# Performance work log

Measured on AMD Instinct MI355X. Metric: run time of the kernel, lower is better.

Reference implementation:

```python
import jax, jax.numpy as jnp
import numpy as np

jax.config.update("jax_enable_x64", True)  # original casts to double for cov/cholesky

B, C, H, W, DR = 64, 2048, 14, 14, 256
EPS = 1e-6      # LCMCOV eps added to covariance diagonal
BN_EPS = 1e-5   # torch BatchNorm2d default eps


def setup_inputs() -> dict:
    key = jax.random.key(0)
    k0, k1 = jax.random.split(key)
    x = jax.random.normal(k0, (B, C, H, W), dtype=jnp.float32)
    # 1x1 conv weight (kaiming fan_out for relu): std = sqrt(2 / fan_out), fan_out = DR*1*1... torch uses fan_out = out_ch*k*k per output; approximate with sqrt(2/C) scale on (DR, C)
    w_conv = jax.random.normal(k1, (DR, C), dtype=jnp.float32) * np.sqrt(2.0 / C).astype(np.float32)
    gamma = jnp.ones((DR,), jnp.float32)
    beta = jnp.zeros((DR,), jnp.float32)
    run_mean = jnp.zeros((DR,), jnp.float32)
    run_var = jnp.ones((DR,), jnp.float32)
    return {"x": x, "w_conv": w_conv, "gamma": gamma, "beta": beta,
            "run_mean": run_mean, "run_var": run_var}


def reference(x, w_conv, gamma, beta, run_mean, run_var):
    b, c, h, w = x.shape
    dr = w_conv.shape[0]
    m = h * w
    # 1x1 conv (no bias) + BatchNorm2d (eval mode, running stats) + ReLU
    y = jnp.einsum('bchw,dc->bdhw', x, w_conv)
    scale = gamma / jnp.sqrt(run_var + BN_EPS)
    y = y * scale[None, :, None, None] + (beta - run_mean * scale)[None, :, None, None]
    y = jax.nn.relu(y)
    # Covpool in float64: x I_hat x^T == (1/M) * (x - mean)(x - mean)^T
    xd = y.reshape(b, dr, m).astype(jnp.float64)
    xc = xd - xd.mean(axis=2, keepdims=True)  # [B, DR, M]
    cov = jnp.einsum('bdm,bem->bde', xc, xc) / m  # [B, DR, DR]
    # LogI_LCM: Cholesky, log the diagonal, symmetrize
    cov = cov + EPS * jnp.eye(dr, dtype=jnp.float64)
    L = jnp.linalg.cholesky(cov)
    diag = jnp.log(jnp.diagonal(L, axis1=-2, axis2=-1))          # [B, DR]
    tril = jnp.tril(L, -1) + jnp.eye(dr, dtype=L.dtype) * diag[:, :, None]
    sym = tril + jnp.swapaxes(tril, -1, -2)
    # Triuvec: upper-triangular (incl diag) entries in row-major order, cast to float32
    iu, ju = jnp.triu_indices(dr)
    return sym[:, iu, ju].astype(jnp.float32)  # [B, DR*(DR+1)/2]
```

## Files before the change

kernel.cpp:

```cpp
#include <hip/hip_runtime.h>
#include <math.h>

#define BB 64
#define CC 2048
#define MM 196
#define DD 256
#define NTOT (BB * MM)

typedef __attribute__((ext_vector_type(8))) short short8;
typedef __attribute__((ext_vector_type(4))) short short4v;
typedef __attribute__((ext_vector_type(4))) unsigned short ushort4v;
typedef __attribute__((ext_vector_type(4))) float f32x4;

__device__ __forceinline__ unsigned short bf16_rne(float f) {
  unsigned int u = __float_as_uint(f);
  unsigned int r = u + 0x7FFFu + ((u >> 16) & 1u);
  return (unsigned short)(r >> 16);
}

__global__ __launch_bounds__(256) void k_prep(
    const float* __restrict__ w, const float* __restrict__ gamma,
    const float* __restrict__ beta, const float* __restrict__ rmean,
    const float* __restrict__ rvar, unsigned short* __restrict__ wh,
    unsigned short* __restrict__ wl, float* __restrict__ sclv,
    float* __restrict__ sftv) {
  const int e0 = (blockIdx.x * 256 + threadIdx.x) * 4;
  f32x4 v = *(const f32x4*)(w + e0);
  ushort4v h, l;
#pragma unroll
  for (int i = 0; i < 4; ++i) {
    unsigned short hb = bf16_rne(v[i]);
    float hf = __uint_as_float((unsigned int)hb << 16);
    h[i] = hb;
    l[i] = bf16_rne(v[i] - hf);
  }
  *(ushort4v*)(wh + e0) = h;
  *(ushort4v*)(wl + e0) = l;
  if (blockIdx.x == 0 && threadIdx.x < DD) {
    int d = threadIdx.x;
    float s = gamma[d] / sqrtf(rvar[d] + 1e-5f);
    sclv[d] = s;
    sftv[d] = beta[d] - rmean[d] * s;
  }
}

__global__ __launch_bounds__(256, 2) void k_conv(
    const float* __restrict__ x, const unsigned short* __restrict__ wh,
    const unsigned short* __restrict__ wl, const float* __restrict__ sclv,
    const float* __restrict__ sftv, float* __restrict__ yt) {
  const int tid = threadIdx.x;
  const int wid = tid >> 6, lane = tid & 63;
  const int quad = lane >> 4, l16 = lane & 15;
  const int n0 = blockIdx.x * 64;

  __shared__ unsigned short Xh[64][36];
  __shared__ unsigned short Xl[64][36];

  f32x4 acc[4][4];
#pragma unroll
  for (int i = 0; i < 4; ++i)
#pragma unroll
    for (int j = 0; j < 4; ++j) acc[i][j] = (f32x4)0.f;

  const int nX = tid & 63, kq = tid >> 6;
  const int gn = n0 + nX;
  const int bX = gn / MM, mX = gn - bX * MM;
  const float* xp = x + (size_t)bX * CC * MM + mX;

  float xr[8];
#pragma unroll
  for (int p = 0; p < 8; ++p) xr[p] = xp[(size_t)(kq * 8 + p) * MM];

  size_t aoff[4];
#pragma unroll
  for (int ds = 0; ds < 4; ++ds)
    aoff[ds] = (size_t)(wid * 64 + ds * 16 + l16) * CC + quad * 8;

  short8 Ah[4], Al[4], Ah2[4], Al2[4];
#pragma unroll
  for (int ds = 0; ds < 4; ++ds) {
    Ah[ds] = *(const short8*)(wh + aoff[ds]);
    Al[ds] = *(const short8*)(wl + aoff[ds]);
  }

  for (int c = 0; c < 64; ++c) {
    const int k0 = c * 32;
    __syncthreads();
    {
      ushort4v h0, h1, l0, l1;
#pragma unroll
      for (int p = 0; p < 4; ++p) {
        unsigned short hb = bf16_rne(xr[p]);
        float hf = __uint_as_float((unsigned int)hb << 16);
        h0[p] = hb;
        l0[p] = bf16_rne(xr[p] - hf);
      }
#pragma unroll
      for (int p = 0; p < 4; ++p) {
        unsigned short hb = bf16_rne(xr[4 + p]);
        float hf = __uint_as_float((unsigned int)hb << 16);
        h1[p] = hb;
        l1[p] = bf16_rne(xr[4 + p] - hf);
      }
      *(ushort4v*)&Xh[nX][kq * 8] = h0;
      *(ushort4v*)&Xh[nX][kq * 8 + 4] = h1;
      *(ushort4v*)&Xl[nX][kq * 8] = l0;
      *(ushort4v*)&Xl[nX][kq * 8 + 4] = l1;
    }
    __syncthreads();
    if (c < 63) {
#pragma unroll
      for (int p = 0; p < 8; ++p)
        xr[p] = xp[(size_t)(k0 + 32 + kq * 8 + p) * MM];
#pragma unroll
      for (int ds = 0; ds < 4; ++ds) {
        Ah2[ds] = *(const short8*)(wh + aoff[ds] + k0 + 32);
        Al2[ds] = *(const short8*)(wl + aoff[ds] + k0 + 32);
      }
    }
#pragma unroll
    for (int ns = 0; ns < 4; ++ns) {
      const unsigned short* bp = &Xh[ns * 16 + l16][quad * 8];
      short4v b0 = *(const short4v*)bp;
      short4v b1 = *(const short4v*)(bp + 4);
      short8 Bh = __builtin_shufflevector(b0, b1, 0, 1, 2, 3, 4, 5, 6, 7);
      const unsigned short* bq = &Xl[ns * 16 + l16][quad * 8];
      short4v c0 = *(const short4v*)bq;
      short4v c1 = *(const short4v*)(bq + 4);
      short8 Bl = __builtin_shufflevector(c0, c1, 0, 1, 2, 3, 4, 5, 6, 7);
#pragma unroll
      for (int ds = 0; ds < 4; ++ds) {
        acc[ds][ns] = __builtin_amdgcn_mfma_f32_16x16x32_bf16(
            Ah[ds], Bh, acc[ds][ns], 0, 0, 0);
        acc[ds][ns] = __builtin_amdgcn_mfma_f32_16x16x32_bf16(
            Ah[ds], Bl, acc[ds][ns], 0, 0, 0);
        acc[ds][ns] = __builtin_amdgcn_mfma_f32_16x16x32_bf16(
            Al[ds], Bh, acc[ds][ns], 0, 0, 0);
      }
    }
#pragma unroll
    for (int ds = 0; ds < 4; ++ds) {
      Ah[ds] = Ah2[ds];
      Al[ds] = Al2[ds];
    }
  }

#pragma unroll
  for (int ds = 0; ds < 4; ++ds) {
    const int dbase = wid * 64 + ds * 16 + quad * 4;
    f32x4 s4 = *(const f32x4*)(sclv + dbase);
    f32x4 f4 = *(const f32x4*)(sftv + dbase);
#pragma unroll
    for (int ns = 0; ns < 4; ++ns) {
      const int n = n0 + ns * 16 + l16;
      const int b = n / MM, m = n - b * MM;
      f32x4 o;
#pragma unroll
      for (int r = 0; r < 4; ++r) {
        float v = fmaf(acc[ds][ns][r], s4[r], f4[r]);
        o[r] = v > 0.f ? v : 0.f;
      }
      *(f32x4*)(yt + ((size_t)b * MM + m) * DD + dbase) = o;
    }
  }
}

__global__ __launch_bounds__(256) void k_means(const float* __restrict__ yt,
                                               double* __restrict__ mean) {
  const int b = blockIdx.x;
  const int d = threadIdx.x;
  const float* p = yt + (size_t)b * MM * DD + d;
  double s0 = 0, s1 = 0, s2 = 0, s3 = 0;
  for (int m = 0; m < MM; m += 4) {
    s0 += (double)p[(size_t)(m + 0) * DD];
    s1 += (double)p[(size_t)(m + 1) * DD];
    s2 += (double)p[(size_t)(m + 2) * DD];
    s3 += (double)p[(size_t)(m + 3) * DD];
  }
  mean[b * DD + d] = (s0 + s1 + s2 + s3) * (1.0 / MM);
}

__global__ __launch_bounds__(256) void k_cov(const float* __restrict__ yt,
                                             const double* __restrict__ mean,
                                             double* __restrict__ cov) {
  const int b = blockIdx.x;
  const int t = blockIdx.y;
  const int ti = (t < 1) ? 0 : (t < 3) ? 1 : (t < 6) ? 2 : 3;
  const int tj = t - (ti * (ti + 1)) / 2;
  const int i0 = ti * 64, j0 = tj * 64;
  const int tid = threadIdx.x;
  const int tx = tid & 15, ty = tid >> 4;

  __shared__ double As[32][66];
  __shared__ double Bs[32][66];

  double acc[4][4];
#pragma unroll
  for (int i = 0; i < 4; ++i)
#pragma unroll
    for (int j = 0; j < 4; ++j) acc[i][j] = 0.0;

  const int dl = tid & 63, kl = tid >> 6;
  const double mA = mean[b * DD + i0 + dl];
  const double mB = mean[b * DD + j0 + dl];
  const float* ybase = yt + (size_t)b * MM * DD;

  for (int k0 = 0; k0 < MM; k0 += 32) {
    __syncthreads();
#pragma unroll
    for (int p = 0; p < 8; ++p) {
      int k = kl + p * 4;
      int m = k0 + k;
      double av = 0.0, bv = 0.0;
      if (m < MM) {
        av = (double)ybase[(size_t)m * DD + i0 + dl] - mA;
        bv = (double)ybase[(size_t)m * DD + j0 + dl] - mB;
      }
      As[k][dl] = av;
      Bs[k][dl] = bv;
    }
    __syncthreads();
#pragma unroll
    for (int k = 0; k < 32; ++k) {
      double a[4], bv[4];
#pragma unroll
      for (int i = 0; i < 4; ++i) a[i] = As[k][ty * 4 + i];
#pragma unroll
      for (int j = 0; j < 4; ++j) bv[j] = Bs[k][tx * 4 + j];
#pragma unroll
      for (int i = 0; i < 4; ++i)
#pragma unroll
        for (int j = 0; j < 4; ++j) acc[i][j] = fma(a[i], bv[j], acc[i][j]);
    }
  }

  double* cb = cov + (size_t)b * DD * DD;
#pragma unroll
  for (int i = 0; i < 4; ++i) {
#pragma unroll
    for (int j = 0; j < 4; ++j) {
      int gi = i0 + ty * 4 + i, gj = j0 + tx * 4 + j;
      double v = acc[i][j] * (1.0 / MM);
      if (gi == gj) v += 1e-6;
      cb[(size_t)gi * DD + gj] = v;
      if (ti != tj) cb[(size_t)gj * DD + gi] = v;
    }
  }
}

__global__ __launch_bounds__(256) void k_panel2(double* __restrict__ cov,
                                                int kb) {
  const int b = blockIdx.x;
  double* A = cov + (size_t)b * DD * DD;
  const int j0 = kb * 32;
  const int tid = threadIdx.x;

  __shared__ double Sp[256][33];
  __shared__ double Lp[224][33];
  __shared__ double L11s[32][33];
  __shared__ double rpivs[32];

  if (blockIdx.y == 0) {
    const int R = DD - j0;
    const int pj = j0 - 32;

    for (int e = tid; e < R * 32; e += 256) {
      int r = e >> 5, c = e & 31;
      Sp[r][c] = A[(size_t)(j0 + r) * DD + j0 + c];
      if (kb > 0) Lp[r][c] = A[(size_t)(j0 + r) * DD + pj + c];
    }
    __syncthreads();

    if (kb > 0) {
      const int cg = tid & 7;
      const int rg = tid >> 3;
      const int c0 = cg * 4;
      for (int r = rg; r < R; r += 32) {
        double a0 = 0, a1 = 0, a2 = 0, a3 = 0;
#pragma unroll
        for (int p = 0; p < 32; ++p) {
          double lr = Lp[r][p];
          a0 = fma(lr, Lp[c0 + 0][p], a0);
          a1 = fma(lr, Lp[c0 + 1][p], a1);
          a2 = fma(lr, Lp[c0 + 2][p], a2);
          a3 = fma(lr, Lp[c0 + 3][p], a3);
        }
        Sp[r][c0 + 0] -= a0;
        Sp[r][c0 + 1] -= a1;
        Sp[r][c0 + 2] -= a2;
        Sp[r][c0 + 3] -= a3;
      }
    }
    __syncthreads();

    if (tid < 32) {
      double r[32];
#pragma unroll
      for (int k = 0; k < 32; ++k) r[k] = Sp[tid][k];
      double rpkeep = 0.0;
#pragma unroll
      for (int j = 0; j < 32; ++j) {
        double dj = __shfl(r[j], j);
        double piv = sqrt(dj);
        double rp = 1.0 / piv;
        if (tid == j) {
          r[j] = piv;
          rpkeep = rp;
        } else {
          r[j] = r[j] * rp;
        }
        double lij = r[j];
#pragma unroll
        for (int k = j + 1; k < 32; ++k) {
          double ck = __shfl(lij, k);
          r[k] -= lij * ck;
        }
      }
#pragma unroll
      for (int k = 0; k < 32; ++k) L11s[tid][k] = (k <= tid) ? r[k] : 0.0;
      rpivs[tid] = rpkeep;
      for (int k = 0; k <= tid; ++k)
        A[(size_t)(j0 + tid) * DD + j0 + k] = r[k];
    }
    __syncthreads();

    const int T = R - 32;
    if (tid < T) {
      double q[32];
#pragma unroll
      for (int k = 0; k < 32; ++k) q[k] = Sp[32 + tid][k];
#pragma unroll
      for (int j = 0; j < 32; ++j) {
        double s = q[j];
#pragma unroll
        for (int k = 0; k < 32; ++k)
          if (k < j) s -= q[k] * L11s[j][k];
        q[j] = s * rpivs[j];
      }
      double* dst = &A[(size_t)(j0 + 32 + tid) * DD + j0];
#pragma unroll
      for (int k = 0; k < 32; ++k) dst[k] = q[k];
    }
  } else {
    const int o = j0 + 32;
    const int S = DD - o;
    const int pj = j0 - 32;
    int tI = 0, tJ = (int)blockIdx.y - 1;
    while (tJ > tI) {
      tJ -= (tI + 1);
      tI++;
    }
    const int i0 = tI * 64, jj0 = tJ * 64;
    const int txl = tid & 15, tyl = tid >> 4;

    double(*Ea)[33] = (double(*)[33])(&Lp[0][0]);
    double(*Eb)[33] = (double(*)[33])(&Lp[64][0]);

    for (int e = tid; e < 64 * 32; e += 256) {
      int r = e >> 5, c = e & 31;
      Ea[r][c] = (i0 + r < S) ? A[(size_t)(o + i0 + r) * DD + pj + c] : 0.0;
      Eb[r][c] = (jj0 + r < S) ? A[(size_t)(o + jj0 + r) * DD + pj + c] : 0.0;
    }
    __syncthreads();

    double s[4][4];
#pragma unroll
    for (int i = 0; i < 4; ++i)
#pragma unroll
      for (int j = 0; j < 4; ++j) s[i][j] = 0.0;

    const int bi = tyl * 4, bj = txl * 4;
#pragma unroll
    for (int k = 0; k < 32; ++k) {
      double a[4], bv[4];
#pragma unroll
      for (int i = 0; i < 4; ++i) a[i] = Ea[bi + i][k];
#pragma unroll
      for (int j = 0; j < 4; ++j) bv[j] = Eb[bj + j][k];
#pragma unroll
      for (int i = 0; i < 4; ++i)
#pragma unroll
        for (int j = 0; j < 4; ++j) s[i][j] = fma(a[i], bv[j], s[i][j]);
    }

#pragma unroll
    for (int i = 0; i < 4; ++i)
#pragma unroll
      for (int j = 0; j < 4; ++j) {
        int gi = i0 + bi + i, gj = jj0 + bj + j;
        if (gi < S && gj < S && gi >= gj)
          A[(size_t)(o + gi) * DD + (o + gj)] -= s[i][j];
      }
  }
}

__global__ __launch_bounds__(256) void k_out(const double* __restrict__ cov,
                                             float* __restrict__ out) {
  const int b = blockIdx.y;
  int t = blockIdx.x;
  int ti = 0, tj = t;
  while (tj >= 4 - ti) {
    tj -= (4 - ti);
    ti++;
  }
  tj += ti;
  const int tid = threadIdx.x;
  const double* A = cov + (size_t)b * DD * DD;

  __shared__ float S[64][65];
  for (int e = tid; e < 4096; e += 256) {
    int jj = e >> 6, ii = e & 63;
    S[jj][ii] = (float)A[(size_t)(tj * 64 + jj) * DD + ti * 64 + ii];
  }
  __syncthreads();

  for (int e = tid; e < 4096; e += 256) {
    int ii = e >> 6, jj = e & 63;
    int i = ti * 64 + ii, j = tj * 64 + jj;
    if (j < i) continue;
    float v = S[jj][ii];
    if (i == j) v = 2.0f * logf(v);
    int off = i * DD - (i * (i - 1)) / 2 + (j - i);
    out[(size_t)b * 32896 + off] = v;
  }
}

extern "C" void kernel_launch(void* const* d_in, const int* in_sizes, int n_in,
                              void* d_out, int out_size, void* d_ws,
                              size_t ws_size, hipStream_t stream) {
  const float* x = (const float*)d_in[0];
  const float* w = (const float*)d_in[1];
  const float* gamma = (const float*)d_in[2];
  const float* beta = (const float*)d_in[3];
  const float* rmean = (const float*)d_in[4];
  const float* rvar = (const float*)d_in[5];
  float* out = (float*)d_out;

  char* ws = (char*)d_ws;
  float* yt = (float*)ws;
  double* mean = (double*)(ws + 12845056);
  double* cov = (double*)(ws + 12845056 + 131072);
  unsigned short* wh = (unsigned short*)cov;
  unsigned short* wl = wh + (DD * CC);
  float* sclv = (float*)(wl + (DD * CC));
  float* sftv = sclv + DD;

  k_prep<<<512, 256, 0, stream>>>(w, gamma, beta, rmean, rvar, wh, wl, sclv,
                                  sftv);
  k_conv<<<NTOT / 64, 256, 0, stream>>>(x, wh, wl, sclv, sftv, yt);
  k_means<<<BB, 256, 0, stream>>>(yt, mean);
  k_cov<<<dim3(BB, 10), 256, 0, stream>>>(yt, mean, cov);
  for (int kb = 0; kb < 8; ++kb) {
    int ntiles = 0;
    if (kb > 0) {
      int S = DD - (kb * 32 + 32);
      if (S > 0) {
        int nt = (S + 63) / 64;
        ntiles = nt * (nt + 1) / 2;
      }
    }
    k_panel2<<<dim3(BB, 1 + ntiles), 256, 0, stream>>>(cov, kb);
  }
  k_out<<<dim3(10, BB), 256, 0, stream>>>(cov, out);
}
```

Baseline: 631.1 us.

## Split conv GEMM along channels and fuse BN/ReLU/mean into reduction kernel

Splits the 1x1 conv GEMM into two channel halves with a smaller 32-column tile, giving four times as many blocks for better GPU fill. Raw partial sums go to two buffers, and a new reduction kernel adds them, applies BN scale/shift and ReLU, and accumulates per-channel means via double atomics. This replaces the separate means kernel. In exchange it adds extra global traffic for the partial buffers and more weight reloads per output.

```diff
diff --git a/kernel.cpp b/kernel.cpp
--- a/kernel.cpp
+++ b/kernel.cpp
@@ -6,6 +6,7 @@
 #define MM 196
 #define DD 256
 #define NTOT (BB * MM)
+#define NT 32
 
 typedef __attribute__((ext_vector_type(8))) short short8;
 typedef __attribute__((ext_vector_type(4))) short short4v;
@@ -23,7 +24,7 @@
     const float* __restrict__ beta, const float* __restrict__ rmean,
     const float* __restrict__ rvar, unsigned short* __restrict__ wh,
     unsigned short* __restrict__ wl, float* __restrict__ sclv,
-    float* __restrict__ sftv) {
+    float* __restrict__ sftv, double* __restrict__ mean) {
   const int e0 = (blockIdx.x * 256 + threadIdx.x) * 4;
   f32x4 v = *(const f32x4*)(w + e0);
   ushort4v h, l;
@@ -42,39 +43,42 @@
     sclv[d] = s;
     sftv[d] = beta[d] - rmean[d] * s;
   }
+  const int gi = blockIdx.x * 256 + threadIdx.x;
+  if (gi < BB * DD) mean[gi] = 0.0;
 }
 
 __global__ __launch_bounds__(256, 2) void k_conv(
     const float* __restrict__ x, const unsigned short* __restrict__ wh,
-    const unsigned short* __restrict__ wl, const float* __restrict__ sclv,
-    const float* __restrict__ sftv, float* __restrict__ yt) {
+    const unsigned short* __restrict__ wl, float* __restrict__ p0,
+    float* __restrict__ p1) {
   const int tid = threadIdx.x;
   const int wid = tid >> 6, lane = tid & 63;
   const int quad = lane >> 4, l16 = lane & 15;
-  const int n0 = blockIdx.x * 64;
-
-  __shared__ unsigned short Xh[64][36];
-  __shared__ unsigned short Xl[64][36];
-
-  f32x4 acc[4][4];
+  const int n0 = blockIdx.x * NT;
+  const int cbase = blockIdx.y * (CC / 2);
+
+  __shared__ unsigned short Xh[NT][36];
+  __shared__ unsigned short Xl[NT][36];
+
+  f32x4 acc[4][2];
 #pragma unroll
   for (int i = 0; i < 4; ++i)
 #pragma unroll
-    for (int j = 0; j < 4; ++j) acc[i][j] = (f32x4)0.f;
-
-  const int nX = tid & 63, kq = tid >> 6;
+    for (int j = 0; j < 2; ++j) acc[i][j] = (f32x4)0.f;
+
+  const int nX = tid & (NT - 1), kq = tid >> 5;
   const int gn = n0 + nX;
   const int bX = gn / MM, mX = gn - bX * MM;
-  const float* xp = x + (size_t)bX * CC * MM + mX;
-
-  float xr[8];
-#pragma unroll
-  for (int p = 0; p < 8; ++p) xr[p] = xp[(size_t)(kq * 8 + p) * MM];
+  const float* xp = x + (size_t)bX * CC * MM + mX + (size_t)cbase * MM;
+
+  float xr[4];
+#pragma unroll
+  for (int p = 0; p < 4; ++p) xr[p] = xp[(size_t)(kq * 4 + p) * MM];
 
   size_t aoff[4];
 #pragma unroll
   for (int ds = 0; ds < 4; ++ds)
-    aoff[ds] = (size_t)(wid * 64 + ds * 16 + l16) * CC + quad * 8;
+    aoff[ds] = (size_t)(wid * 64 + ds * 16 + l16) * CC + cbase + quad * 8;
 
   short8 Ah[4], Al[4], Ah2[4], Al2[4];
 #pragma unroll
@@ -83,11 +87,11 @@
     Al[ds] = *(const short8*)(wl + aoff[ds]);
   }
 
-  for (int c = 0; c < 64; ++c) {
+  for (int c = 0; c < 32; ++c) {
     const int k0 = c * 32;
     __syncthreads();
     {
-      ushort4v h0, h1, l0, l1;
+      ushort4v h0, l0;
 #pragma unroll
       for (int p = 0; p < 4; ++p) {
         unsigned short hb = bf16_rne(xr[p]);
@@ -95,23 +99,14 @@
         h0[p] = hb;
         l0[p] = bf16_rne(xr[p] - hf);
       }
-#pragma unroll
-      for (int p = 0; p < 4; ++p) {
-        unsigned short hb = bf16_rne(xr[4 + p]);
-        float hf = __uint_as_float((unsigned int)hb << 16);
-        h1[p] = hb;
-        l1[p] = bf16_rne(xr[4 + p] - hf);
-      }
-      *(ushort4v*)&Xh[nX][kq * 8] = h0;
-      *(ushort4v*)&Xh[nX][kq * 8 + 4] = h1;
-      *(ushort4v*)&Xl[nX][kq * 8] = l0;
-      *(ushort4v*)&Xl[nX][kq * 8 + 4] = l1;
-    }
-    __syncthreads();
-    if (c < 63) {
-#pragma unroll
-      for (int p = 0; p < 8; ++p)
-        xr[p] = xp[(size_t)(k0 + 32 + kq * 8 + p) * MM];
+      *(ushort4v*)&Xh[nX][kq * 4] = h0;
+      *(ushort4v*)&Xl[nX][kq * 4] = l0;
+    }
+    __syncthreads();
+    if (c < 31) {
+#pragma unroll
+      for (int p = 0; p < 4; ++p)
+        xr[p] = xp[(size_t)(k0 + 32 + kq * 4 + p) * MM];
 #pragma unroll
       for (int ds = 0; ds < 4; ++ds) {
         Ah2[ds] = *(const short8*)(wh + aoff[ds] + k0 + 32);
@@ -119,7 +114,7 @@
       }
     }
 #pragma unroll
-    for (int ns = 0; ns < 4; ++ns) {
+    for (int ns = 0; ns < 2; ++ns) {
       const unsigned short* bp = &Xh[ns * 16 + l16][quad * 8];
       short4v b0 = *(const short4v*)bp;
       short4v b1 = *(const short4v*)(bp + 4);
@@ -145,39 +140,41 @@
     }
   }
 
+  float* dst = (blockIdx.y == 0) ? p0 : p1;
 #pragma unroll
   for (int ds = 0; ds < 4; ++ds) {
     const int dbase = wid * 64 + ds * 16 + quad * 4;
-    f32x4 s4 = *(const f32x4*)(sclv + dbase);
-    f32x4 f4 = *(const f32x4*)(sftv + dbase);
-#pragma unroll
-    for (int ns = 0; ns < 4; ++ns) {
+#pragma unroll
+    for (int ns = 0; ns < 2; ++ns) {
       const int n = n0 + ns * 16 + l16;
       const int b = n / MM, m = n - b * MM;
-      f32x4 o;
-#pragma unroll
-      for (int r = 0; r < 4; ++r) {
-        float v = fmaf(acc[ds][ns][r], s4[r], f4[r]);
-        o[r] = v > 0.f ? v : 0.f;
-      }
-      *(f32x4*)(yt + ((size_t)b * MM + m) * DD + dbase) = o;
-    }
-  }
-}
-
-__global__ __launch_bounds__(256) void k_means(const float* __restrict__ yt,
-                                               double* __restrict__ mean) {
+      *(f32x4*)(dst + ((size_t)b * MM + m) * DD + dbase) = acc[ds][ns];
+    }
+  }
+}
+
+__global__ __launch_bounds__(256) void k_red(float* __restrict__ yt,
+                                             const float* __restrict__ p1,
+                                             const float* __restrict__ sclv,
+                                             const float* __restrict__ sftv,
+                                             double* __restrict__ mean) {
   const int b = blockIdx.x;
+  const int m0 = blockIdx.y * 28;
   const int d = threadIdx.x;
-  const float* p = yt + (size_t)b * MM * DD + d;
-  double s0 = 0, s1 = 0, s2 = 0, s3 = 0;
-  for (int m = 0; m < MM; m += 4) {
-    s0 += (double)p[(size_t)(m + 0) * DD];
-    s1 += (double)p[(size_t)(m + 1) * DD];
-    s2 += (double)p[(size_t)(m + 2) * DD];
-    s3 += (double)p[(size_t)(m + 3) * DD];
-  }
-  mean[b * DD + d] = (s0 + s1 + s2 + s3) * (1.0 / MM);
+  const float s = sclv[d];
+  const float f = sftv[d];
+  const size_t base = ((size_t)b * MM + m0) * DD + d;
+  double sum = 0.0;
+#pragma unroll 4
+  for (int m = 0; m < 28; ++m) {
+    const size_t idx = base + (size_t)m * DD;
+    float v = yt[idx] + p1[idx];
+    v = fmaf(v, s, f);
+    v = v > 0.f ? v : 0.f;
+    yt[idx] = v;
+    sum += (double)v;
+  }
+  atomicAdd(mean + b * DD + d, sum * (1.0 / MM));
 }
 
 __global__ __launch_bounds__(256) void k_cov(const float* __restrict__ yt,
@@ -444,11 +441,12 @@
   unsigned short* wl = wh + (DD * CC);
   float* sclv = (float*)(wl + (DD * CC));
   float* sftv = sclv + DD;
+  float* part1 = (float*)((char*)cov + 2099200);
 
   k_prep<<<512, 256, 0, stream>>>(w, gamma, beta, rmean, rvar, wh, wl, sclv,
-                                  sftv);
-  k_conv<<<NTOT / 64, 256, 0, stream>>>(x, wh, wl, sclv, sftv, yt);
-  k_means<<<BB, 256, 0, stream>>>(yt, mean);
+                                  sftv, mean);
+  k_conv<<<dim3(NTOT / NT, 2), 256, 0, stream>>>(x, wh, wl, yt, part1);
+  k_red<<<dim3(BB, 7), 256, 0, stream>>>(yt, part1, sclv, sftv, mean);
   k_cov<<<dim3(BB, 10), 256, 0, stream>>>(yt, mean, cov);
   for (int kb = 0; kb < 8; ++kb) {
     int ntiles = 0;
```

New measurement: 651.4 us. +3.2%, slower.

## Fuse blocked Cholesky panels, trailing updates and output into one per-batch kernel

Applied to the files above, without the earlier changes.

The eight per-panel launches of the blocked Cholesky and the separate output kernel are replaced by a single kernel with one block per batch matrix. The block loops over the panels, keeps the freshly solved panel in shared memory and reuses it for a right-looking trailing update done serially over tiles, then writes the log-diagonal triangular output itself. This removes launch overhead, the global round-trips for panel reloads and the lazy previous-panel update. In exchange, only 64 blocks run for the whole factorization, so trailing-tile parallelism across workgroups is lost and the GPU is heavily underused during this phase.

```diff
diff --git a/kernel.cpp b/kernel.cpp
--- a/kernel.cpp
+++ b/kernel.cpp
@@ -248,55 +248,31 @@
   }
 }
 
-__global__ __launch_bounds__(256) void k_panel2(double* __restrict__ cov,
-                                                int kb) {
+__global__ __launch_bounds__(256) void k_chol(double* __restrict__ cov,
+                                              float* __restrict__ out) {
   const int b = blockIdx.x;
+  const int tid = threadIdx.x;
   double* A = cov + (size_t)b * DD * DD;
-  const int j0 = kb * 32;
-  const int tid = threadIdx.x;
-
-  __shared__ double Sp[256][33];
-  __shared__ double Lp[224][33];
+
+  __shared__ double Lb[256][33];
   __shared__ double L11s[32][33];
   __shared__ double rpivs[32];
-
-  if (blockIdx.y == 0) {
+  float* Sf = (float*)&Lb[0][0];
+
+  for (int kb = 0; kb < 8; ++kb) {
+    const int j0 = kb * 32;
     const int R = DD - j0;
-    const int pj = j0 - 32;
-
+    __syncthreads();
     for (int e = tid; e < R * 32; e += 256) {
       int r = e >> 5, c = e & 31;
-      Sp[r][c] = A[(size_t)(j0 + r) * DD + j0 + c];
-      if (kb > 0) Lp[r][c] = A[(size_t)(j0 + r) * DD + pj + c];
-    }
-    __syncthreads();
-
-    if (kb > 0) {
-      const int cg = tid & 7;
-      const int rg = tid >> 3;
-      const int c0 = cg * 4;
-      for (int r = rg; r < R; r += 32) {
-        double a0 = 0, a1 = 0, a2 = 0, a3 = 0;
-#pragma unroll
-        for (int p = 0; p < 32; ++p) {
-          double lr = Lp[r][p];
-          a0 = fma(lr, Lp[c0 + 0][p], a0);
-          a1 = fma(lr, Lp[c0 + 1][p], a1);
-          a2 = fma(lr, Lp[c0 + 2][p], a2);
-          a3 = fma(lr, Lp[c0 + 3][p], a3);
-        }
-        Sp[r][c0 + 0] -= a0;
-        Sp[r][c0 + 1] -= a1;
-        Sp[r][c0 + 2] -= a2;
-        Sp[r][c0 + 3] -= a3;
-      }
+      Lb[r][c] = A[(size_t)(j0 + r) * DD + j0 + c];
     }
     __syncthreads();
 
     if (tid < 32) {
       double r[32];
 #pragma unroll
-      for (int k = 0; k < 32; ++k) r[k] = Sp[tid][k];
+      for (int k = 0; k < 32; ++k) r[k] = Lb[tid][k];
       double rpkeep = 0.0;
 #pragma unroll
       for (int j = 0; j < 32; ++j) {
@@ -319,16 +295,16 @@
 #pragma unroll
       for (int k = 0; k < 32; ++k) L11s[tid][k] = (k <= tid) ? r[k] : 0.0;
       rpivs[tid] = rpkeep;
-      for (int k = 0; k <= tid; ++k)
-        A[(size_t)(j0 + tid) * DD + j0 + k] = r[k];
-    }
-    __syncthreads();
-
-    const int T = R - 32;
-    if (tid < T) {
+#pragma unroll
+      for (int k = 0; k < 32; ++k)
+        if (k <= tid) A[(size_t)(j0 + tid) * DD + j0 + k] = r[k];
+    }
+    __syncthreads();
+
+    if (tid >= 32 && tid < R) {
       double q[32];
 #pragma unroll
-      for (int k = 0; k < 32; ++k) q[k] = Sp[32 + tid][k];
+      for (int k = 0; k < 32; ++k) q[k] = Lb[tid][k];
 #pragma unroll
       for (int j = 0; j < 32; ++j) {
         double s = q[j];
@@ -337,91 +313,95 @@
           if (k < j) s -= q[k] * L11s[j][k];
         q[j] = s * rpivs[j];
       }
-      double* dst = &A[(size_t)(j0 + 32 + tid) * DD + j0];
-#pragma unroll
-      for (int k = 0; k < 32; ++k) dst[k] = q[k];
-    }
-  } else {
+      double* dst = &A[(size_t)(j0 + tid) * DD + j0];
+#pragma unroll
+      for (int k = 0; k < 32; ++k) {
+        dst[k] = q[k];
+        Lb[tid][k] = q[k];
+      }
+    }
+    __syncthreads();
+
     const int o = j0 + 32;
     const int S = DD - o;
-    const int pj = j0 - 32;
-    int tI = 0, tJ = (int)blockIdx.y - 1;
-    while (tJ > tI) {
-      tJ -= (tI + 1);
-      tI++;
-    }
-    const int i0 = tI * 64, jj0 = tJ * 64;
-    const int txl = tid & 15, tyl = tid >> 4;
-
-    double(*Ea)[33] = (double(*)[33])(&Lp[0][0]);
-    double(*Eb)[33] = (double(*)[33])(&Lp[64][0]);
-
-    for (int e = tid; e < 64 * 32; e += 256) {
-      int r = e >> 5, c = e & 31;
-      Ea[r][c] = (i0 + r < S) ? A[(size_t)(o + i0 + r) * DD + pj + c] : 0.0;
-      Eb[r][c] = (jj0 + r < S) ? A[(size_t)(o + jj0 + r) * DD + pj + c] : 0.0;
-    }
-    __syncthreads();
-
-    double s[4][4];
-#pragma unroll
-    for (int i = 0; i < 4; ++i)
-#pragma unroll
-      for (int j = 0; j < 4; ++j) s[i][j] = 0.0;
-
-    const int bi = tyl * 4, bj = txl * 4;
-#pragma unroll
-    for (int k = 0; k < 32; ++k) {
-      double a[4], bv[4];
-#pragma unroll
-      for (int i = 0; i < 4; ++i) a[i] = Ea[bi + i][k];
-#pragma unroll
-      for (int j = 0; j < 4; ++j) bv[j] = Eb[bj + j][k];
-#pragma unroll
-      for (int i = 0; i < 4; ++i)
-#pragma unroll
-        for (int j = 0; j < 4; ++j) s[i][j] = fma(a[i], bv[j], s[i][j]);
-    }
-
-#pragma unroll
-    for (int i = 0; i < 4; ++i)
-#pragma unroll
-      for (int j = 0; j < 4; ++j) {
-        int gi = i0 + bi + i, gj = jj0 + bj + j;
-        if (gi < S && gj < S && gi >= gj)
-          A[(size_t)(o + gi) * DD + (o + gj)] -= s[i][j];
-      }
-  }
-}
-
-__global__ __launch_bounds__(256) void k_out(const double* __restrict__ cov,
-                                             float* __restrict__ out) {
-  const int b = blockIdx.y;
-  int t = blockIdx.x;
-  int ti = 0, tj = t;
-  while (tj >= 4 - ti) {
-    tj -= (4 - ti);
-    ti++;
-  }
-  tj += ti;
-  const int tid = threadIdx.x;
-  const double* A = cov + (size_t)b * DD * DD;
-
-  __shared__ float S[64][65];
-  for (int e = tid; e < 4096; e += 256) {
-    int jj = e >> 6, ii = e & 63;
-    S[jj][ii] = (float)A[(size_t)(tj * 64 + jj) * DD + ti * 64 + ii];
-  }
-  __syncthreads();
-
-  for (int e = tid; e < 4096; e += 256) {
-    int ii = e >> 6, jj = e & 63;
-    int i = ti * 64 + ii, j = tj * 64 + jj;
-    if (j < i) continue;
-    float v = S[jj][ii];
-    if (i == j) v = 2.0f * logf(v);
-    int off = i * DD - (i * (i - 1)) / 2 + (j - i);
-    out[(size_t)b * 32896 + off] = v;
+    if (S > 0) {
+      const int nt = (S + 63) / 64;
+      const int ntiles = nt * (nt + 1) / 2;
+      const int txl = tid & 15, tyl = tid >> 4;
+      const int bi = tyl * 4, bj = txl * 4;
+      for (int tt = 0; tt < ntiles; ++tt) {
+        int tI = 0, tJ = tt;
+        while (tJ > tI) {
+          tJ -= (tI + 1);
+          tI++;
+        }
+        const int i0 = tI * 64, jj0 = tJ * 64;
+
+        int rA[4], rB[4];
+        bool va[4], vb[4];
+#pragma unroll
+        for (int i = 0; i < 4; ++i) {
+          int g = i0 + bi + i;
+          va[i] = g < S;
+          rA[i] = 32 + (va[i] ? g : 0);
+          int h = jj0 + bj + i;
+          vb[i] = h < S;
+          rB[i] = 32 + (vb[i] ? h : 0);
+        }
+
+        double s[4][4];
+#pragma unroll
+        for (int i = 0; i < 4; ++i)
+#pragma unroll
+          for (int j = 0; j < 4; ++j) s[i][j] = 0.0;
+
+#pragma unroll
+        for (int k = 0; k < 32; ++k) {
+          double a[4], bv[4];
+#pragma unroll
+          for (int i = 0; i < 4; ++i) a[i] = va[i] ? Lb[rA[i]][k] : 0.0;
+#pragma unroll
+          for (int j = 0; j < 4; ++j) bv[j] = vb[j] ? Lb[rB[j]][k] : 0.0;
+#pragma unroll
+          for (int i = 0; i < 4; ++i)
+#pragma unroll
+            for (int j = 0; j < 4; ++j) s[i][j] = fma(a[i], bv[j], s[i][j]);
+        }
+
+#pragma unroll
+        for (int i = 0; i < 4; ++i)
+#pragma unroll
+          for (int j = 0; j < 4; ++j) {
+            int gi = i0 + bi + i, gj = jj0 + bj + j;
+            if (gi < S && gj < S && gi >= gj)
+              A[(size_t)(o + gi) * DD + (o + gj)] -= s[i][j];
+          }
+      }
+    }
+  }
+
+  for (int t = 0; t < 10; ++t) {
+    int ti = 0, tj = t;
+    while (tj >= 4 - ti) {
+      tj -= (4 - ti);
+      ti++;
+    }
+    tj += ti;
+    __syncthreads();
+    for (int e = tid; e < 4096; e += 256) {
+      int jj = e >> 6, ii = e & 63;
+      Sf[jj * 65 + ii] = (float)A[(size_t)(tj * 64 + jj) * DD + ti * 64 + ii];
+    }
+    __syncthreads();
+    for (int e = tid; e < 4096; e += 256) {
+      int ii = e >> 6, jj = e & 63;
+      int i = ti * 64 + ii, j = tj * 64 + jj;
+      if (j < i) continue;
+      float v = Sf[jj * 65 + ii];
+      if (i == j) v = 2.0f * logf(v);
+      int off = i * DD - (i * (i - 1)) / 2 + (j - i);
+      out[(size_t)b * 32896 + off] = v;
+    }
   }
 }
 
@@ -450,16 +430,5 @@
   k_conv<<<NTOT / 64, 256, 0, stream>>>(x, wh, wl, sclv, sftv, yt);
   k_means<<<BB, 256, 0, stream>>>(yt, mean);
   k_cov<<<dim3(BB, 10), 256, 0, stream>>>(yt, mean, cov);
-  for (int kb = 0; kb < 8; ++kb) {
-    int ntiles = 0;
-    if (kb > 0) {
-      int S = DD - (kb * 32 + 32);
-      if (S > 0) {
-        int nt = (S + 63) / 64;
-        ntiles = nt * (nt + 1) / 2;
-      }
-    }
-    k_panel2<<<dim3(BB, 1 + ntiles), 256, 0, stream>>>(cov, kb);
-  }
-  k_out<<<dim3(10, BB), 256, 0, stream>>>(cov, out);
-}
+  k_chol<<<BB, 256, 0, stream>>>(cov, out);
+}
```

Measured after the change: 931.4 us. 1.48x slower.

## Keep Cholesky panel rows in registers and fuse output extraction into last panel

Applied to the files above, without the earlier changes.

The panel kernel now has each thread hold one row of the diagonal-block panel and one row of the previous panel in registers instead of staging the whole panel in LDS. The shared footprint shrinks to a single reused buffer. The separate output kernel is folded into the final panel launch (kb==7), which removes one launch. The trade-off is heavy register pressure from two 32-double arrays per thread, and the output extraction for each batch element now runs in a single block.

```diff
diff --git a/kernel.cpp b/kernel.cpp
--- a/kernel.cpp
+++ b/kernel.cpp
@@ -248,98 +248,121 @@
   }
 }
 
-__global__ __launch_bounds__(256) void k_panel2(double* __restrict__ cov,
+__global__ __launch_bounds__(256) void k_panel3(double* __restrict__ cov,
+                                                float* __restrict__ out,
                                                 int kb) {
   const int b = blockIdx.x;
   double* A = cov + (size_t)b * DD * DD;
   const int j0 = kb * 32;
   const int tid = threadIdx.x;
 
-  __shared__ double Sp[256][33];
-  __shared__ double Lp[224][33];
-  __shared__ double L11s[32][33];
-  __shared__ double rpivs[32];
+  __shared__ double sh[4224];
 
   if (blockIdx.y == 0) {
+    double(*LpTop)[33] = (double(*)[33])sh;
+    double(*L11s)[33] = (double(*)[33])(sh + 1056);
+    double* rpivs = sh + 2112;
     const int R = DD - j0;
     const int pj = j0 - 32;
 
-    for (int e = tid; e < R * 32; e += 256) {
-      int r = e >> 5, c = e & 31;
-      Sp[r][c] = A[(size_t)(j0 + r) * DD + j0 + c];
-      if (kb > 0) Lp[r][c] = A[(size_t)(j0 + r) * DD + pj + c];
-    }
-    __syncthreads();
+    double sp[32];
+    const double* rowp = A + (size_t)(j0 + tid) * DD;
+    if (tid < R) {
+#pragma unroll
+      for (int c = 0; c < 32; ++c) sp[c] = rowp[j0 + c];
+    }
 
     if (kb > 0) {
-      const int cg = tid & 7;
-      const int rg = tid >> 3;
-      const int c0 = cg * 4;
-      for (int r = rg; r < R; r += 32) {
-        double a0 = 0, a1 = 0, a2 = 0, a3 = 0;
-#pragma unroll
-        for (int p = 0; p < 32; ++p) {
-          double lr = Lp[r][p];
-          a0 = fma(lr, Lp[c0 + 0][p], a0);
-          a1 = fma(lr, Lp[c0 + 1][p], a1);
-          a2 = fma(lr, Lp[c0 + 2][p], a2);
-          a3 = fma(lr, Lp[c0 + 3][p], a3);
-        }
-        Sp[r][c0 + 0] -= a0;
-        Sp[r][c0 + 1] -= a1;
-        Sp[r][c0 + 2] -= a2;
-        Sp[r][c0 + 3] -= a3;
-      }
-    }
-    __syncthreads();
+      double lp[32];
+      if (tid < R) {
+#pragma unroll
+        for (int c = 0; c < 32; ++c) lp[c] = rowp[pj + c];
+      }
+      if (tid < 32) {
+#pragma unroll
+        for (int c = 0; c < 32; ++c) LpTop[tid][c] = lp[c];
+      }
+      __syncthreads();
+      if (tid < R) {
+#pragma unroll
+        for (int c = 0; c < 32; ++c) {
+          double a = 0.0;
+#pragma unroll
+          for (int p = 0; p < 32; ++p) a = fma(lp[p], LpTop[c][p], a);
+          sp[c] -= a;
+        }
+      }
+    }
 
     if (tid < 32) {
-      double r[32];
-#pragma unroll
-      for (int k = 0; k < 32; ++k) r[k] = Sp[tid][k];
       double rpkeep = 0.0;
 #pragma unroll
       for (int j = 0; j < 32; ++j) {
-        double dj = __shfl(r[j], j);
+        double dj = __shfl(sp[j], j);
         double piv = sqrt(dj);
         double rp = 1.0 / piv;
         if (tid == j) {
-          r[j] = piv;
+          sp[j] = piv;
           rpkeep = rp;
         } else {
-          r[j] = r[j] * rp;
-        }
-        double lij = r[j];
+          sp[j] = sp[j] * rp;
+        }
+        double lij = sp[j];
 #pragma unroll
         for (int k = j + 1; k < 32; ++k) {
           double ck = __shfl(lij, k);
-          r[k] -= lij * ck;
-        }
-      }
-#pragma unroll
-      for (int k = 0; k < 32; ++k) L11s[tid][k] = (k <= tid) ? r[k] : 0.0;
+          sp[k] -= lij * ck;
+        }
+      }
+#pragma unroll
+      for (int k = 0; k < 32; ++k) L11s[tid][k] = (k <= tid) ? sp[k] : 0.0;
       rpivs[tid] = rpkeep;
       for (int k = 0; k <= tid; ++k)
-        A[(size_t)(j0 + tid) * DD + j0 + k] = r[k];
-    }
-    __syncthreads();
-
-    const int T = R - 32;
-    if (tid < T) {
-      double q[32];
-#pragma unroll
-      for (int k = 0; k < 32; ++k) q[k] = Sp[32 + tid][k];
+        A[(size_t)(j0 + tid) * DD + j0 + k] = sp[k];
+    }
+    __syncthreads();
+
+    if (tid >= 32 && tid < R) {
 #pragma unroll
       for (int j = 0; j < 32; ++j) {
-        double s = q[j];
+        double s = sp[j];
 #pragma unroll
         for (int k = 0; k < 32; ++k)
-          if (k < j) s -= q[k] * L11s[j][k];
-        q[j] = s * rpivs[j];
-      }
-      double* dst = &A[(size_t)(j0 + 32 + tid) * DD + j0];
-#pragma unroll
-      for (int k = 0; k < 32; ++k) dst[k] = q[k];
+          if (k < j) s -= sp[k] * L11s[j][k];
+        sp[j] = s * rpivs[j];
+      }
+      double* dst = A + (size_t)(j0 + tid) * DD + j0;
+#pragma unroll
+      for (int k = 0; k < 32; ++k) dst[k] = sp[k];
+    }
+
+    if (kb == 7) {
+      float* Sf = (float*)sh;
+      __syncthreads();
+      for (int t = 0; t < 10; ++t) {
+        int ti = 0, tj = t;
+        while (tj >= 4 - ti) {
+          tj -= (4 - ti);
+          ti++;
+        }
+        tj += ti;
+        __syncthreads();
+        for (int e = tid; e < 4096; e += 256) {
+          int jj = e >> 6, ii = e & 63;
+          Sf[jj * 65 + ii] =
+              (float)A[(size_t)(tj * 64 + jj) * DD + ti * 64 + ii];
+        }
+        __syncthreads();
+        for (int e = tid; e < 4096; e += 256) {
+          int ii = e >> 6, jj = e & 63;
+          int i = ti * 64 + ii, j = tj * 64 + jj;
+          if (j < i) continue;
+          float v = Sf[jj * 65 + ii];
+          if (i == j) v = 2.0f * logf(v);
+          int off = i * DD - (i * (i - 1)) / 2 + (j - i);
+          out[(size_t)b * 32896 + off] = v;
+        }
+      }
     }
   } else {
     const int o = j0 + 32;
@@ -353,8 +376,8 @@
     const int i0 = tI * 64, jj0 = tJ * 64;
     const int txl = tid & 15, tyl = tid >> 4;
 
-    double(*Ea)[33] = (double(*)[33])(&Lp[0][0]);
-    double(*Eb)[33] = (double(*)[33])(&Lp[64][0]);
+    double(*Ea)[33] = (double(*)[33])sh;
+    double(*Eb)[33] = (double(*)[33])(sh + 2112);
 
     for (int e = tid; e < 64 * 32; e += 256) {
       int r = e >> 5, c = e & 31;
@@ -391,37 +414,6 @@
         if (gi < S && gj < S && gi >= gj)
           A[(size_t)(o + gi) * DD + (o + gj)] -= s[i][j];
       }
-  }
-}
-
-__global__ __launch_bounds__(256) void k_out(const double* __restrict__ cov,
-                                             float* __restrict__ out) {
-  const int b = blockIdx.y;
-  int t = blockIdx.x;
-  int ti = 0, tj = t;
-  while (tj >= 4 - ti) {
-    tj -= (4 - ti);
-    ti++;
-  }
-  tj += ti;
-  const int tid = threadIdx.x;
-  const double* A = cov + (size_t)b * DD * DD;
-
-  __shared__ float S[64][65];
-  for (int e = tid; e < 4096; e += 256) {
-    int jj = e >> 6, ii = e & 63;
-    S[jj][ii] = (float)A[(size_t)(tj * 64 + jj) * DD + ti * 64 + ii];
-  }
-  __syncthreads();
-
-  for (int e = tid; e < 4096; e += 256) {
-    int ii = e >> 6, jj = e & 63;
-    int i = ti * 64 + ii, j = tj * 64 + jj;
-    if (j < i) continue;
-    float v = S[jj][ii];
-    if (i == j) v = 2.0f * logf(v);
-    int off = i * DD - (i * (i - 1)) / 2 + (j - i);
-    out[(size_t)b * 32896 + off] = v;
   }
 }
 
@@ -459,7 +451,6 @@
         ntiles = nt * (nt + 1) / 2;
       }
     }
-    k_panel2<<<dim3(BB, 1 + ntiles), 256, 0, stream>>>(cov, kb);
-  }
-  k_out<<<dim3(10, BB), 256, 0, stream>>>(cov, out);
-}
+    k_panel3<<<dim3(BB, 1 + ntiles), 256, 0, stream>>>(cov, out, kb);
+  }
+}
```

New measurement: 639.2 us. About the same (+1.3%).
